# Optimization experiments

Measured on AMD Instinct MI355X. Metric: run time of the kernel, lower is better.

Reference implementation:

```python
import jax, jax.numpy as jnp
import numpy as np

B, M, D = 8, 1024, 768          # batch, tokens, model dim
N, P = 32, 32                   # experts, slots per expert (N*P == M)
K = 8                           # mix_k (router top-k)
H = 2048                        # expert MLP hidden dim
EPS = 1e-12


def setup_inputs() -> dict:
    key = jax.random.key(0)
    ks = jax.random.split(key, 6)
    std_d = 1.0 / np.sqrt(D)
    std_h = 1.0 / np.sqrt(H)
    return {
        "x": jax.random.normal(ks[0], (B, M, D), jnp.float32),
        "cluster_assignments": jax.random.randint(ks[1], (B, M, K), 0, N),
        "phi": jax.random.normal(ks[2], (D, N, P), jnp.float32) * std_d,
        "scale": jnp.ones((1,), jnp.float32),
        "w1": jax.random.normal(ks[3], (N, D, H), jnp.float32) * std_d,
        "b1": jnp.zeros((N, H), jnp.float32),
        "w2": jax.random.normal(ks[4], (N, H, D), jnp.float32) * std_h,
        "b2": jnp.zeros((N, D), jnp.float32),
    }


def _seg_mean(vals, idx, num_segments):
    # index_reduce(..., 'mean', include_self=False): empty segments stay 0
    s = jax.ops.segment_sum(vals, idx, num_segments=num_segments)
    c = jax.ops.segment_sum(jnp.ones((vals.shape[0], 1), vals.dtype), idx,
                            num_segments=num_segments)
    return jnp.where(c > 0, s / jnp.maximum(c, 1.0), 0.0)


def _compute_acmoe(x_flat, top_assign):
    # MAD-based per-cluster, per-dim scaling (mad=True, mix_weights=False)
    mean_kd = _seg_mean(x_flat, top_assign, N)                 # [N, D]
    centered = jnp.abs(x_flat - mean_kd[top_assign])           # [B*M, D]
    w_mad = _seg_mean(centered, top_assign, N)                 # [N, D]
    W = 1.0 / (w_mad + 0.35)
    top_clamp = 5.0 * W.mean()
    W = jnp.minimum(W, top_clamp)
    W = W / W.mean()
    return W[top_assign]                                       # [B*M, D]


def reference(x, cluster_assignments, phi, scale, w1, b1, w2, b2):
    # normalize tokens (dim=2) and phi (dim=0), scale phi
    xn = x / jnp.maximum(jnp.linalg.norm(x, axis=-1, keepdims=True), EPS)
    phin = scale * phi / jnp.maximum(jnp.linalg.norm(phi, axis=0, keepdims=True), EPS)

    # ACMoE feature re-weighting (no-grad in original)
    top_assign = cluster_assignments.reshape(-1, K)[:, 0]       # [B*M]
    Mw = jax.lax.stop_gradient(_compute_acmoe(
        jax.lax.stop_gradient(xn.reshape(-1, D)), top_assign))
    xn = (xn.reshape(-1, D) * Mw).reshape(B, M, D)

    logits = jnp.einsum('bmd,dnp->bmnp', xn, phin)              # [B,M,N,P]
    aff = logits.reshape(B, M, N * P)
    mixing_weights, slot_assignments = jax.lax.top_k(aff, K)    # [B,M,K]
    new_clusters = slot_assignments // P

    disp = jax.nn.softmax(logits, axis=1)                       # over tokens m
    comb = jax.nn.softmax(aff, axis=-1).reshape(B, M, N, P)     # over (n,p)

    xs = jnp.einsum('bmd,bmnp->bnpd', xn, disp)                 # [B,N,P,D]
    # per-expert MLP, batched over expert axis n
    h = jnp.einsum('bnpd,ndh->bnph', xs, w1) + b1[None, :, None, :]
    h = jax.nn.gelu(h, approximate=False)
    ys = jnp.einsum('bnph,nhd->bnpd', h, w2) + b2[None, :, None, :]

    y = jnp.einsum('bnpd,bmnp->bmd', ys, comb)                  # [B,M,D]
    return y, mixing_weights, new_clusters
```

## Files before the change

### kernel.cpp

```cpp
#include <hip/hip_runtime.h>
#include <cmath>

#define NB    8
#define MTOK  1024
#define BMT   8192
#define DD    768
#define NEXP  32
#define PSLOT 32
#define NP    1024
#define KTOP  8
#define HH    2048

#define SLICES 128
#define TPS    64

typedef unsigned short ushort;
typedef __attribute__((ext_vector_type(8))) short short8v;
typedef __attribute__((ext_vector_type(4))) short short4v;
typedef __attribute__((ext_vector_type(4))) float f32x4;

__device__ __forceinline__ ushort bf16_rne(float x) {
    unsigned u = __float_as_uint(x);
    unsigned r = (u + 0x7FFFu + ((u >> 16) & 1u)) >> 16;
    return (ushort)r;
}
__device__ __forceinline__ float bf16_to_f(ushort h) {
    return __uint_as_float(((unsigned)h) << 16);
}
__device__ __forceinline__ void split2(float x, ushort& hi, ushort& lo) {
    hi = bf16_rne(x);
    lo = bf16_rne(x - bf16_to_f(hi));
}
__device__ __forceinline__ unsigned cvt_pk_bf16(float a, float b) {
    unsigned r;
    asm volatile("v_cvt_pk_bf16_f32 %0, %1, %2" : "=v"(r) : "v"(a), "v"(b));
    return r;
}

__device__ __forceinline__ void gl_lds16(const ushort* g, ushort* l) {
    __builtin_amdgcn_global_load_lds(
        (const __attribute__((address_space(1))) void*)g,
        (__attribute__((address_space(3))) void*)l, 16, 0, 0);
}

__global__ __launch_bounds__(256) void norm_x(const float* __restrict__ x, float* __restrict__ xn) {
    int tok = blockIdx.x;
    int t = threadIdx.x;
    const float* p = x + (long)tok * DD;
    float v0 = p[t], v1 = p[t + 256], v2 = p[t + 512];
    float ss = v0 * v0 + v1 * v1 + v2 * v2;
#pragma unroll
    for (int o = 32; o; o >>= 1) ss += __shfl_xor(ss, o);
    __shared__ float sred[4];
    if ((t & 63) == 0) sred[t >> 6] = ss;
    __syncthreads();
    ss = sred[0] + sred[1] + sred[2] + sred[3];
    float inv = 1.0f / fmaxf(sqrtf(ss), 1e-12f);
    float* q = xn + (long)tok * DD;
    q[t] = v0 * inv; q[t + 256] = v1 * inv; q[t + 512] = v2 * inv;
}

__global__ __launch_bounds__(256) void norm_phi_T(const float* __restrict__ phi, const float* __restrict__ scale,
                                                  ushort* __restrict__ phT_hi, ushort* __restrict__ phT_lo) {
    int np = blockIdx.x;
    int t = threadIdx.x;
    float ss = 0.f;
    for (int d = t; d < DD; d += 256) {
        float v = phi[(long)d * NP + np];
        ss += v * v;
    }
#pragma unroll
    for (int o = 32; o; o >>= 1) ss += __shfl_xor(ss, o);
    __shared__ float sred[4];
    if ((t & 63) == 0) sred[t >> 6] = ss;
    __syncthreads();
    ss = sred[0] + sred[1] + sred[2] + sred[3];
    float sc = scale[0] / fmaxf(sqrtf(ss), 1e-12f);
    for (int d = t; d < DD; d += 256) {
        float v = phi[(long)d * NP + np] * sc;
        ushort h, l; split2(v, h, l);
        phT_hi[(long)np * DD + d] = h;
        phT_lo[(long)np * DD + d] = l;
    }
}

__global__ __launch_bounds__(256) void cluster_sum(const float* __restrict__ xn, const int* __restrict__ ca,
                                                   float* __restrict__ spart, float* __restrict__ cntpart) {
    __shared__ float s[NEXP][256];
    __shared__ float cnt[NEXP];
    int chunk = blockIdx.x, slice = blockIdx.y, t = threadIdx.x;
#pragma unroll
    for (int n = 0; n < NEXP; ++n) s[n][t] = 0.f;
    if (t < NEXP) cnt[t] = 0.f;
    __syncthreads();
    int tok0 = slice * TPS;
    for (int i = 0; i < TPS; ++i) {
        int tok = tok0 + i;
        int a = ca[tok * KTOP];
        float v = xn[(long)tok * DD + chunk * 256 + t];
        s[a][t] += v;
        if (chunk == 0 && t == 0) cnt[a] += 1.f;
    }
    __syncthreads();
    for (int n = 0; n < NEXP; ++n)
        spart[(long)slice * (NEXP * DD) + n * DD + chunk * 256 + t] = s[n][t];
    if (chunk == 0 && t < NEXP) cntpart[slice * NEXP + t] = cnt[t];
}

__global__ __launch_bounds__(256) void reduce_parts(const float* __restrict__ part, float* __restrict__ outv,
                                                    const float* __restrict__ cntpart, float* __restrict__ ccnt,
                                                    int doCnt) {
    int i = blockIdx.x * 256 + threadIdx.x;
    float s = 0.f;
#pragma unroll 8
    for (int sl = 0; sl < SLICES; ++sl) s += part[(long)sl * (NEXP * DD) + i];
    outv[i] = s;
    if (doCnt && i < NEXP) {
        float c = 0.f;
#pragma unroll 8
        for (int sl = 0; sl < SLICES; ++sl) c += cntpart[sl * NEXP + i];
        ccnt[i] = c;
    }
}

__global__ __launch_bounds__(256) void cluster_mad(const float* __restrict__ xn, const int* __restrict__ ca,
                                                   const float* __restrict__ csum, const float* __restrict__ ccnt,
                                                   float* __restrict__ mpart) {
    __shared__ float md[NEXP][256];
    __shared__ float mean[NEXP][256];
    int chunk = blockIdx.x, slice = blockIdx.y, t = threadIdx.x;
#pragma unroll
    for (int n = 0; n < NEXP; ++n) {
        float c = ccnt[n];
        mean[n][t] = (c > 0.f) ? csum[n * DD + chunk * 256 + t] / c : 0.f;
        md[n][t] = 0.f;
    }
    __syncthreads();
    int tok0 = slice * TPS;
    for (int i = 0; i < TPS; ++i) {
        int tok = tok0 + i;
        int a = ca[tok * KTOP];
        float v = xn[(long)tok * DD + chunk * 256 + t];
        md[a][t] += fabsf(v - mean[a][t]);
    }
    __syncthreads();
    for (int n = 0; n < NEXP; ++n)
        mpart[(long)slice * (NEXP * DD) + n * DD + chunk * 256 + t] = md[n][t];
}

__global__ __launch_bounds__(1024) void compute_W(const float* __restrict__ cmad, const float* __restrict__ ccnt,
                                                  float* __restrict__ W) {
    __shared__ float s[16];
    int t = threadIdx.x;
    auto block_sum = [&](float v) -> float {
#pragma unroll
        for (int o = 32; o; o >>= 1) v += __shfl_xor(v, o);
        if ((t & 63) == 0) s[t >> 6] = v;
        __syncthreads();
        float tot = 0.f;
#pragma unroll
        for (int i = 0; i < 16; ++i) tot += s[i];
        __syncthreads();
        return tot;
    };
    const int TOT = NEXP * DD;
    float p = 0.f;
    for (int i = t; i < TOT; i += 1024) {
        int n = i / DD;
        float c = ccnt[n];
        float wm = (c > 0.f) ? cmad[i] / c : 0.f;
        p += 1.f / (wm + 0.35f);
    }
    float mean1 = block_sum(p) / (float)TOT;
    float clamp = 5.f * mean1;
    p = 0.f;
    for (int i = t; i < TOT; i += 1024) {
        int n = i / DD;
        float c = ccnt[n];
        float wm = (c > 0.f) ? cmad[i] / c : 0.f;
        p += fminf(1.f / (wm + 0.35f), clamp);
    }
    float mean2 = block_sum(p) / (float)TOT;
    float inv2 = 1.f / mean2;
    for (int i = t; i < TOT; i += 1024) {
        int n = i / DD;
        float c = ccnt[n];
        float wm = (c > 0.f) ? cmad[i] / c : 0.f;
        W[i] = fminf(1.f / (wm + 0.35f), clamp) * inv2;
    }
}

__global__ __launch_bounds__(192) void apply_W(float* __restrict__ xn, const int* __restrict__ ca,
                                               const float* __restrict__ W,
                                               ushort* __restrict__ hi, ushort* __restrict__ lo) {
    int tok = blockIdx.x;
    long d4 = (long)tok * DD + threadIdx.x * 4;
    int a = ca[tok * KTOP];
    float4 v = *reinterpret_cast<float4*>(xn + d4);
    float4 w = *reinterpret_cast<const float4*>(W + a * DD + threadIdx.x * 4);
    v.x *= w.x; v.y *= w.y; v.z *= w.z; v.w *= w.w;
    *reinterpret_cast<float4*>(xn + d4) = v;
    ushort h0,h1,h2,h3,l0,l1,l2,l3;
    split2(v.x,h0,l0); split2(v.y,h1,l1); split2(v.z,h2,l2); split2(v.w,h3,l3);
    *reinterpret_cast<short4v*>(hi + d4) = short4v{(short)h0,(short)h1,(short)h2,(short)h3};
    *reinterpret_cast<short4v*>(lo + d4) = short4v{(short)l0,(short)l1,(short)l2,(short)l3};
}

template <bool F32>
__global__ __launch_bounds__(256) void make_T(const void* __restrict__ srcv, ushort* __restrict__ dst,
                                              int R, int C) {
    __shared__ ushort tile[64][65];
    int z = blockIdx.z;
    int c0 = blockIdx.x * 64, r0 = blockIdx.y * 64;
    int tr = threadIdx.x >> 4;
    int tc4 = (threadIdx.x & 15) * 4;
    long base = (long)z * R * C;
#pragma unroll
    for (int i = 0; i < 4; ++i) {
        int r = tr + i * 16;
        if constexpr (F32) {
            const float* s = (const float*)srcv;
            float4 v = *reinterpret_cast<const float4*>(s + base + (long)(r0 + r) * C + c0 + tc4);
            tile[r][tc4 + 0] = bf16_rne(v.x); tile[r][tc4 + 1] = bf16_rne(v.y);
            tile[r][tc4 + 2] = bf16_rne(v.z); tile[r][tc4 + 3] = bf16_rne(v.w);
        } else {
            const ushort* s = (const ushort*)srcv;
            short4v v = *reinterpret_cast<const short4v*>(s + base + (long)(r0 + r) * C + c0 + tc4);
            tile[r][tc4 + 0] = (ushort)v.x; tile[r][tc4 + 1] = (ushort)v.y;
            tile[r][tc4 + 2] = (ushort)v.z; tile[r][tc4 + 3] = (ushort)v.w;
        }
    }
    __syncthreads();
#pragma unroll
    for (int i = 0; i < 4; ++i) {
        int oc = tr + i * 16;
        short4v o = short4v{(short)tile[tc4 + 0][oc], (short)tile[tc4 + 1][oc],
                            (short)tile[tc4 + 2][oc], (short)tile[tc4 + 3][oc]};
        *reinterpret_cast<short4v*>(dst + base + (long)(c0 + oc) * R + r0 + tc4) = o;
    }
}

template <int MODE, int AMAP, int EPI, bool CBF16, int CMAP>
__global__ __launch_bounds__(256) void gemm2(
    const ushort* __restrict__ Ah_g, const ushort* __restrict__ Al_g,
    const float*  __restrict__ Bf_g,
    const ushort* __restrict__ Bh_g, const ushort* __restrict__ Bl_g,
    float* __restrict__ Cf, ushort* __restrict__ Cb,
    int K, int lda, int ldb, int ldc,
    long sA, long sB, long sC,
    const float* __restrict__ bias, int biasStride) {
    constexpr bool PAIR = (MODE == 1);
    constexpr int BUFS = PAIR ? 12288 : 8192;
    constexpr int BM   = PAIR ? 64 : 128;
    constexpr int MI   = PAIR ? 2 : 4;
    __shared__ __attribute__((aligned(16))) ushort lds[3 * BUFS];

    int orig = blockIdx.x + gridDim.x * (blockIdx.y + gridDim.y * blockIdx.z);
    int nwg = gridDim.x * gridDim.y * gridDim.z;
    int wg = (orig & 7) * (nwg >> 3) + (orig >> 3);
    int bx = wg % gridDim.x;
    int rest = wg / gridDim.x;
    int by = rest % gridDim.y;
    int z  = rest / gridDim.y;
    const int m0 = by * BM;
    const int n0 = bx * 128;

    const int tid = threadIdx.x, lane = tid & 63, w = tid >> 6;
    const int wr = w >> 1, wc = w & 1;
    const int lr = lane & 15, kh = lane >> 4;

    const int NCA = PAIR ? 1 : 2;
    long arowA[2]; int kOffA[2];
#pragma unroll
    for (int i = 0; i < NCA; ++i) {
        int c = i * 256 + tid;
        int r = c >> 2, sp = c & 3;
        kOffA[i] = (sp ^ ((r >> 1) & 3)) << 3;
        int rg = m0 + r;
        if constexpr (AMAP == 0) arowA[i] = (long)z * sA + (long)rg * lda;
        else arowA[i] = ((long)(rg >> 5) * 1024 + (long)z * 32 + (rg & 31)) * (long)lda;
    }
    long browB[2]; int kOffB[2];
#pragma unroll
    for (int i = 0; i < 2; ++i) {
        int c = i * 256 + tid;
        int r = c >> 2, sp = c & 3;
        kOffB[i] = (sp ^ ((r >> 1) & 3)) << 3;
        browB[i] = (long)z * sB + (long)(n0 + r) * ldb;
    }
    const int kq = tid & 7, nq = tid >> 3;

    f32x4 acc[MI][4];
#pragma unroll
    for (int i = 0; i < MI; ++i)
#pragma unroll
        for (int j = 0; j < 4; ++j) acc[i][j] = (f32x4)(0.f);

    auto stageA = [&](int buf, int kk0) {
        const int bb = buf * BUFS;
        if constexpr (MODE == 1) {
            gl_lds16(Ah_g + arowA[0] + kk0 + kOffA[0], &lds[bb + (w * 64) * 8]);
            gl_lds16(Al_g + arowA[0] + kk0 + kOffA[0], &lds[bb + 2048 + (w * 64) * 8]);
#pragma unroll
            for (int i = 0; i < 2; ++i) {
                int base = bb + 4096 + (i * 256 + w * 64) * 8;
                gl_lds16(Bh_g + browB[i] + kk0 + kOffB[i], &lds[base]);
                gl_lds16(Bl_g + browB[i] + kk0 + kOffB[i], &lds[base + 4096]);
            }
        } else if constexpr (MODE == 0) {
#pragma unroll
            for (int i = 0; i < 2; ++i)
                gl_lds16(Ah_g + arowA[i] + kk0 + kOffA[i], &lds[bb + (i * 256 + w * 64) * 8]);
#pragma unroll
            for (int i = 0; i < 2; ++i)
                gl_lds16(Bh_g + browB[i] + kk0 + kOffB[i], &lds[bb + 4096 + (i * 256 + w * 64) * 8]);
        } else {
#pragma unroll
            for (int i = 0; i < 2; ++i)
                gl_lds16(Ah_g + arowA[i] + kk0 + kOffA[i], &lds[bb + (i * 256 + w * 64) * 8]);
        }
    };

    auto loadB = [&](float4 (&rB)[4], int kk0) {
#pragma unroll
        for (int dk = 0; dk < 4; ++dk)
            rB[dk] = *reinterpret_cast<const float4*>(
                Bf_g + (long)z * sB + (long)(kk0 + kq * 4 + dk) * ldb + n0 + nq * 4);
    };

    auto bwrite = [&](int buf, float4 (&rB)[4]) {
        unsigned p0[4], p1[4];
        p0[0] = cvt_pk_bf16(rB[0].x, rB[1].x); p1[0] = cvt_pk_bf16(rB[2].x, rB[3].x);
        p0[1] = cvt_pk_bf16(rB[0].y, rB[1].y); p1[1] = cvt_pk_bf16(rB[2].y, rB[3].y);
        p0[2] = cvt_pk_bf16(rB[0].z, rB[1].z); p1[2] = cvt_pk_bf16(rB[2].z, rB[3].z);
        p0[3] = cvt_pk_bf16(rB[0].w, rB[1].w); p1[3] = cvt_pk_bf16(rB[2].w, rB[3].w);
#pragma unroll
        for (int dn = 0; dn < 4; ++dn) {
            int n = nq * 4 + dn;
            int phys = (kq >> 1) ^ ((n >> 1) & 3);
            int off = buf * BUFS + 4096 + n * 32 + phys * 8 + (kq & 1) * 4;
            *reinterpret_cast<uint2*>(&lds[off]) = make_uint2(p0[dn], p1[dn]);
        }
    };

    auto compute = [&](int buf) {
        const int aB = buf * BUFS;
        const int bB = buf * BUFS + 4096;
        short8v bh[4], bl[4];
#pragma unroll
        for (int nj = 0; nj < 4; ++nj) {
            int rb = wc * 64 + nj * 16 + lr;
            int off = bB + rb * 32 + ((kh ^ ((rb >> 1) & 3)) << 3);
            bh[nj] = *reinterpret_cast<const short8v*>(&lds[off]);
            if constexpr (PAIR) bl[nj] = *reinterpret_cast<const short8v*>(&lds[off + 4096]);
        }
        __builtin_amdgcn_s_setprio(1);
#pragma unroll
        for (int mi = 0; mi < MI; ++mi) {
            int ra = wr * (PAIR ? 32 : 64) + mi * 16 + lr;
            int off = aB + ra * 32 + ((kh ^ ((ra >> 1) & 3)) << 3);
            short8v ah = *reinterpret_cast<const short8v*>(&lds[off]);
            if constexpr (PAIR) {
                short8v al = *reinterpret_cast<const short8v*>(&lds[off + 2048]);
#pragma unroll
                for (int nj = 0; nj < 4; ++nj) {
                    acc[mi][nj] = __builtin_amdgcn_mfma_f32_16x16x32_bf16(ah, bh[nj], acc[mi][nj], 0, 0, 0);
                    acc[mi][nj] = __builtin_amdgcn_mfma_f32_16x16x32_bf16(ah, bl[nj], acc[mi][nj], 0, 0, 0);
                    acc[mi][nj] = __builtin_amdgcn_mfma_f32_16x16x32_bf16(al, bh[nj], acc[mi][nj], 0, 0, 0);
                }
            } else {
#pragma unroll
                for (int nj = 0; nj < 4; ++nj)
                    acc[mi][nj] = __builtin_amdgcn_mfma_f32_16x16x32_bf16(ah, bh[nj], acc[mi][nj], 0, 0, 0);
            }
        }
        __builtin_amdgcn_s_setprio(0);
    };

    const int nt = K >> 5;
    if constexpr (MODE == 0 || MODE == 1) {
        stageA(0, 0);
        stageA(1, 32);
        if constexpr (MODE == 1) { asm volatile("s_waitcnt vmcnt(6)" ::: "memory"); }
        else                     { asm volatile("s_waitcnt vmcnt(4)" ::: "memory"); }
        __builtin_amdgcn_s_barrier();
        __builtin_amdgcn_sched_barrier(0);
        int cc = 0, cn2 = 2;
        for (int t = 0; t < nt; ++t) {
            bool deep = (t + 2 < nt);
            if (deep) stageA(cn2, (t + 2) << 5);
            compute(cc);
            if (deep) {
                if constexpr (MODE == 1) { asm volatile("s_waitcnt vmcnt(6)" ::: "memory"); }
                else                     { asm volatile("s_waitcnt vmcnt(4)" ::: "memory"); }
            } else {
                asm volatile("s_waitcnt vmcnt(0)" ::: "memory");
            }
            if (t + 1 < nt) {
                __builtin_amdgcn_s_barrier();
                __builtin_amdgcn_sched_barrier(0);
            }
            cc = (cc == 2) ? 0 : cc + 1;
            cn2 = (cn2 == 2) ? 0 : cn2 + 1;
        }
    } else {
        float4 rBa[4], rBb[4];
        loadB(rBa, 0);
        bwrite(0, rBa);
        stageA(0, 0);
        stageA(1, 32);
        loadB(rBb, 32);
        asm volatile("s_waitcnt vmcnt(6) lgkmcnt(0)" ::: "memory");
        __builtin_amdgcn_s_barrier();
        __builtin_amdgcn_sched_barrier(0);
        int cc = 0, cn1 = 1, cn2 = 2;
        auto iter = [&](int t, float4 (&ld)[4], float4 (&wr_)[4]) {
            bool deep = (t + 2 < nt);
            if (deep) { stageA(cn2, (t + 2) << 5); loadB(ld, (t + 2) << 5); }
            compute(cc);
            if (t + 1 < nt) bwrite(cn1, wr_);
            if (deep) { asm volatile("s_waitcnt vmcnt(6) lgkmcnt(0)" ::: "memory"); }
            else      { asm volatile("s_waitcnt vmcnt(0) lgkmcnt(0)" ::: "memory"); }
            if (t + 1 < nt) {
                __builtin_amdgcn_s_barrier();
                __builtin_amdgcn_sched_barrier(0);
            }
            cc = (cc == 2) ? 0 : cc + 1;
            cn1 = (cn1 == 2) ? 0 : cn1 + 1;
            cn2 = (cn2 == 2) ? 0 : cn2 + 1;
        };
        for (int t = 0; t < nt; t += 2) {
            iter(t, rBa, rBb);
            iter(t + 1, rBb, rBa);
        }
    }

#pragma unroll
    for (int mi = 0; mi < MI; ++mi)
#pragma unroll
        for (int j = 0; j < 4; ++j) {
            int rg = m0 + wr * (PAIR ? 32 : 64) + mi * 16 + kh * 4 + j;
            long roff;
            if constexpr (CMAP == 1) roff = ((long)(rg >> 5) * 1024 + (long)z * 32 + (rg & 31)) * (long)ldc;
            else                     roff = (long)z * sC + (long)rg * ldc;
#pragma unroll
            for (int nj = 0; nj < 4; ++nj) {
                int col = n0 + wc * 64 + nj * 16 + lr;
                float v = acc[mi][nj][j];
                if constexpr (EPI >= 1) v += bias[(long)z * biasStride + col];
                if constexpr (EPI == 2) v = 0.5f * v * (1.0f + erff(v * 0.70710678118654752f));
                if constexpr (CBF16) Cb[roff + col] = bf16_rne(v);
                else                 Cf[roff + col] = v;
            }
        }
}

__global__ __launch_bounds__(64) void row_topk(const float* __restrict__ logits,
                                               float* __restrict__ mix_out, float* __restrict__ clus_out,
                                               ushort* __restrict__ comb) {
    int row = blockIdx.x;
    int lane = threadIdx.x;
    const float* p = logits + (long)row * NP;
    float v[16];
#pragma unroll
    for (int i = 0; i < 16; ++i) v[i] = p[lane + i * 64];
    float mx = v[0];
#pragma unroll
    for (int i = 1; i < 16; ++i) mx = fmaxf(mx, v[i]);
#pragma unroll
    for (int o = 32; o; o >>= 1) mx = fmaxf(mx, __shfl_xor(mx, o));
    float s = 0.f;
#pragma unroll
    for (int i = 0; i < 16; ++i) s += __expf(v[i] - mx);
#pragma unroll
    for (int o = 32; o; o >>= 1) s += __shfl_xor(s, o);
    float inv = 1.0f / s;
    ushort* crow = comb + (long)row * NP;
#pragma unroll
    for (int i = 0; i < 16; ++i)
        crow[lane + i * 64] = bf16_rne(__expf(v[i] - mx) * inv);
#pragma unroll
    for (int k = 0; k < KTOP; ++k) {
        float bv = -INFINITY; int bi = 1 << 30;
#pragma unroll
        for (int i = 0; i < 16; ++i) {
            if (v[i] > bv) { bv = v[i]; bi = lane + i * 64; }
        }
#pragma unroll
        for (int o = 32; o; o >>= 1) {
            float ov = __shfl_xor(bv, o); int oi = __shfl_xor(bi, o);
            if (ov > bv || (ov == bv && oi < bi)) { bv = ov; bi = oi; }
        }
        int owner = bi & 63, slot = bi >> 6;
        if (lane == owner) {
#pragma unroll
            for (int i = 0; i < 16; ++i) if (slot == i) v[i] = -INFINITY;
        }
        if (lane == k) {
            mix_out[(long)row * KTOP + k] = bv;
            clus_out[(long)row * KTOP + k] = (float)(bi >> 5);
        }
    }
}

__global__ __launch_bounds__(256) void col_stats_part(const float* __restrict__ logits,
                                                      float* __restrict__ pmax, float* __restrict__ psum) {
    int b = blockIdx.z, ms = blockIdx.y, npc = blockIdx.x;
    int np = npc * 256 + threadIdx.x;
    const float* p = logits + ((long)b * MTOK + ms * 128) * NP + np;
    float mx = -INFINITY, s = 0.f;
    for (int m = 0; m < 128; ++m) {
        float v = p[(long)m * NP];
        float nm = fmaxf(mx, v);
        s = s * __expf(mx - nm) + __expf(v - nm);
        mx = nm;
    }
    long o = ((long)b * 8 + ms) * NP + np;
    pmax[o] = mx; psum[o] = s;
}

__global__ __launch_bounds__(256) void make_dispT(const float* __restrict__ logits,
                                                  const float* __restrict__ pmax, const float* __restrict__ psum,
                                                  ushort* __restrict__ dispT) {
    __shared__ float tile[64][65];
    __shared__ float smax[64], sinv[64];
    int b = blockIdx.z, np0 = blockIdx.x * 64, m0 = blockIdx.y * 64;
    int tr = threadIdx.x >> 6, tc = threadIdx.x & 63;
    if (threadIdx.x < 64) {
        int np = np0 + threadIdx.x;
        float mx = -INFINITY;
#pragma unroll
        for (int ms = 0; ms < 8; ++ms) mx = fmaxf(mx, pmax[((long)b * 8 + ms) * NP + np]);
        float s = 0.f;
#pragma unroll
        for (int ms = 0; ms < 8; ++ms) {
            long o = ((long)b * 8 + ms) * NP + np;
            s += psum[o] * __expf(pmax[o] - mx);
        }
        smax[threadIdx.x] = mx;
        sinv[threadIdx.x] = 1.0f / s;
    }
    const float* src = logits + ((long)b * MTOK + m0) * NP + np0;
#pragma unroll
    for (int i = 0; i < 16; ++i) {
        int m = tr * 16 + i;
        tile[m][tc] = src[(long)m * NP + tc];
    }
    __syncthreads();
#pragma unroll
    for (int i = 0; i < 16; ++i) {
        int npl = tr * 16 + i;
        float v = __expf(tile[tc][npl] - smax[npl]) * sinv[npl];
        dispT[((long)b * NP + np0 + npl) * MTOK + (m0 + tc)] = bf16_rne(v);
    }
}

extern "C" void kernel_launch(void* const* d_in, const int* in_sizes, int n_in,
                              void* d_out, int out_size, void* d_ws, size_t ws_size,
                              hipStream_t stream) {
    const float* x    = (const float*)d_in[0];
    const int*   ca   = (const int*)d_in[1];
    const float* phi  = (const float*)d_in[2];
    const float* scale= (const float*)d_in[3];
    const float* w1   = (const float*)d_in[4];
    const float* b1   = (const float*)d_in[5];
    const float* w2   = (const float*)d_in[6];
    const float* b2   = (const float*)d_in[7];
    float* out = (float*)d_out;
    float* ws  = (float*)d_ws;

    float*  xn       = ws;
    float*  logits   = xn + 6291456;
    ushort* xnp_hi   = (ushort*)(logits + 8388608);
    ushort* xnp_lo   = xnp_hi + 6291456;
    ushort* phT_hi   = xnp_lo + 6291456;
    ushort* phT_lo   = phT_hi + 786432;
    ushort* dispT_bf = phT_lo + 786432;
    ushort* comb_bf  = dispT_bf + 8388608;
    ushort* xs_bf    = comb_bf + 8388608;
    ushort* h_bf     = xs_bf + 6291456;
    ushort* xnT_bf   = h_bf + 16777216;
    ushort* ysT_bf   = xnT_bf + 6291456;
    float*  stats    = (float*)(ysT_bf + 6291456);
    float* pmax      = stats;
    float* psum      = pmax + 65536;
    float* csum      = psum + 65536;
    float* cmad      = csum + 24576;
    float* Wbuf      = cmad + 24576;
    float* ccnt      = Wbuf + 24576;
    float* cntpart   = ccnt + 64;
    float* spart     = cntpart + 4096;
    float* mpart     = spart + 3145728;
    float* ys        = xn;

    float* out_y    = out;
    float* out_mix  = out + 6291456;
    float* out_clus = out + 6291456 + 65536;

    norm_x<<<BMT, 256, 0, stream>>>(x, xn);
    norm_phi_T<<<NP, 256, 0, stream>>>(phi, scale, phT_hi, phT_lo);

    cluster_sum<<<dim3(3, SLICES), 256, 0, stream>>>(xn, ca, spart, cntpart);
    reduce_parts<<<96, 256, 0, stream>>>(spart, csum, cntpart, ccnt, 1);
    cluster_mad<<<dim3(3, SLICES), 256, 0, stream>>>(xn, ca, csum, ccnt, mpart);
    reduce_parts<<<96, 256, 0, stream>>>(mpart, cmad, nullptr, nullptr, 0);
    compute_W<<<1, 1024, 0, stream>>>(cmad, ccnt, Wbuf);
    apply_W<<<BMT, 192, 0, stream>>>(xn, ca, Wbuf, xnp_hi, xnp_lo);

    make_T<false><<<dim3(12, 16, NB), 256, 0, stream>>>(xnp_hi, xnT_bf, MTOK, DD);

    gemm2<1, 0, 0, false, 0><<<dim3(8, 128, 1), 256, 0, stream>>>(
        xnp_hi, xnp_lo, nullptr, phT_hi, phT_lo, logits, nullptr,
        DD, DD, DD, NP, 0, 0, 0, nullptr, 0);

    row_topk<<<BMT, 64, 0, stream>>>(logits, out_mix, out_clus, comb_bf);
    col_stats_part<<<dim3(4, 8, NB), 256, 0, stream>>>(logits, pmax, psum);
    make_dispT<<<dim3(16, 16, NB), 256, 0, stream>>>(logits, pmax, psum, dispT_bf);

    gemm2<0, 0, 0, true, 0><<<dim3(6, 8, NB), 256, 0, stream>>>(
        dispT_bf, nullptr, nullptr, xnT_bf, nullptr, nullptr, xs_bf,
        MTOK, MTOK, MTOK, DD,
        (long)NP * MTOK, (long)DD * MTOK, (long)NP * DD, nullptr, 0);

    gemm2<2, 1, 2, true, 0><<<dim3(16, 2, NEXP), 256, 0, stream>>>(
        xs_bf, nullptr, w1, nullptr, nullptr, nullptr, h_bf,
        DD, DD, HH, HH,
        0, (long)DD * HH, (long)256 * HH, b1, HH);

    gemm2<2, 0, 1, false, 1><<<dim3(6, 2, NEXP), 256, 0, stream>>>(
        h_bf, nullptr, w2, nullptr, nullptr, ys, nullptr,
        HH, HH, DD, DD,
        (long)256 * HH, (long)HH * DD, 0, b2, DD);

    make_T<true><<<dim3(12, 16, NB), 256, 0, stream>>>(ys, ysT_bf, MTOK, DD);

    gemm2<0, 0, 0, false, 0><<<dim3(6, 8, NB), 256, 0, stream>>>(
        comb_bf, nullptr, nullptr, ysT_bf, nullptr, out_y, nullptr,
        NP, NP, NP, DD,
        (long)MTOK * NP, (long)DD * NP, (long)MTOK * DD, nullptr, 0);
}
```

Before: 478.4 us.

## Double M tile to 256 rows with 512-thread blocks in bf16 GEMMs

For the non-paired GEMM modes, the workgroup grows to 512 threads and covers 256 output rows instead of 128. Each B tile staged in LDS is now shared by twice as many rows, which halves B traffic per output and halves the grid size. B staging and fp32→bf16 conversion are remapped to the new thread count, the vmcnt waits are adjusted, and the s_setprio hints around the MFMA loop are dropped. The trade-off is fewer workgroups: some launches fall to 192 blocks, which can leave CUs idle, and the larger blocks limit occupancy.

```diff
diff --git a/kernel.cpp b/kernel.cpp
--- a/kernel.cpp
+++ b/kernel.cpp
@@ -241,7 +241,7 @@
 }
 
 template <int MODE, int AMAP, int EPI, bool CBF16, int CMAP>
-__global__ __launch_bounds__(256) void gemm2(
+__global__ __launch_bounds__((MODE == 1) ? 256 : 512) void gemm2(
     const ushort* __restrict__ Ah_g, const ushort* __restrict__ Al_g,
     const float*  __restrict__ Bf_g,
     const ushort* __restrict__ Bh_g, const ushort* __restrict__ Bl_g,
@@ -250,8 +250,10 @@
     long sA, long sB, long sC,
     const float* __restrict__ bias, int biasStride) {
     constexpr bool PAIR = (MODE == 1);
-    constexpr int BUFS = PAIR ? 12288 : 8192;
-    constexpr int BM   = PAIR ? 64 : 128;
+    constexpr int THR  = PAIR ? 256 : 512;
+    constexpr int BUFS = 12288;
+    constexpr int BOFF = PAIR ? 4096 : 8192;
+    constexpr int BM   = PAIR ? 64 : 256;
     constexpr int MI   = PAIR ? 2 : 4;
     __shared__ __attribute__((aligned(16))) ushort lds[3 * BUFS];
 
@@ -273,7 +275,7 @@
     long arowA[2]; int kOffA[2];
 #pragma unroll
     for (int i = 0; i < NCA; ++i) {
-        int c = i * 256 + tid;
+        int c = i * THR + tid;
         int r = c >> 2, sp = c & 3;
         kOffA[i] = (sp ^ ((r >> 1) & 3)) << 3;
         int rg = m0 + r;
@@ -284,11 +286,13 @@
 #pragma unroll
     for (int i = 0; i < 2; ++i) {
         int c = i * 256 + tid;
-        int r = c >> 2, sp = c & 3;
-        kOffB[i] = (sp ^ ((r >> 1) & 3)) << 3;
-        browB[i] = (long)z * sB + (long)(n0 + r) * ldb;
-    }
-    const int kq = tid & 7, nq = tid >> 3;
+        if (c < 512) {
+            int r = c >> 2, sp = c & 3;
+            kOffB[i] = (sp ^ ((r >> 1) & 3)) << 3;
+            browB[i] = (long)z * sB + (long)(n0 + r) * ldb;
+        }
+    }
+    const int kqh = tid & 15, nq = tid >> 4;
 
     f32x4 acc[MI][4];
 #pragma unroll
@@ -310,42 +314,42 @@
         } else if constexpr (MODE == 0) {
 #pragma unroll
             for (int i = 0; i < 2; ++i)
-                gl_lds16(Ah_g + arowA[i] + kk0 + kOffA[i], &lds[bb + (i * 256 + w * 64) * 8]);
+                gl_lds16(Ah_g + arowA[i] + kk0 + kOffA[i], &lds[bb + (i * THR + w * 64) * 8]);
+            gl_lds16(Bh_g + browB[0] + kk0 + kOffB[0], &lds[bb + BOFF + (w * 64) * 8]);
+        } else {
 #pragma unroll
             for (int i = 0; i < 2; ++i)
-                gl_lds16(Bh_g + browB[i] + kk0 + kOffB[i], &lds[bb + 4096 + (i * 256 + w * 64) * 8]);
-        } else {
-#pragma unroll
-            for (int i = 0; i < 2; ++i)
-                gl_lds16(Ah_g + arowA[i] + kk0 + kOffA[i], &lds[bb + (i * 256 + w * 64) * 8]);
+                gl_lds16(Ah_g + arowA[i] + kk0 + kOffA[i], &lds[bb + (i * THR + w * 64) * 8]);
         }
     };
 
-    auto loadB = [&](float4 (&rB)[4], int kk0) {
-#pragma unroll
-        for (int dk = 0; dk < 4; ++dk)
+    auto loadB = [&](float4 (&rB)[2], int kk0) {
+#pragma unroll
+        for (int dk = 0; dk < 2; ++dk)
             rB[dk] = *reinterpret_cast<const float4*>(
-                Bf_g + (long)z * sB + (long)(kk0 + kq * 4 + dk) * ldb + n0 + nq * 4);
+                Bf_g + (long)z * sB + (long)(kk0 + kqh * 2 + dk) * ldb + n0 + nq * 4);
     };
 
-    auto bwrite = [&](int buf, float4 (&rB)[4]) {
-        unsigned p0[4], p1[4];
-        p0[0] = cvt_pk_bf16(rB[0].x, rB[1].x); p1[0] = cvt_pk_bf16(rB[2].x, rB[3].x);
-        p0[1] = cvt_pk_bf16(rB[0].y, rB[1].y); p1[1] = cvt_pk_bf16(rB[2].y, rB[3].y);
-        p0[2] = cvt_pk_bf16(rB[0].z, rB[1].z); p1[2] = cvt_pk_bf16(rB[2].z, rB[3].z);
-        p0[3] = cvt_pk_bf16(rB[0].w, rB[1].w); p1[3] = cvt_pk_bf16(rB[2].w, rB[3].w);
+    auto bwrite = [&](int buf, float4 (&rB)[2]) {
+        unsigned p[4];
+        p[0] = cvt_pk_bf16(rB[0].x, rB[1].x);
+        p[1] = cvt_pk_bf16(rB[0].y, rB[1].y);
+        p[2] = cvt_pk_bf16(rB[0].z, rB[1].z);
+        p[3] = cvt_pk_bf16(rB[0].w, rB[1].w);
+        int k = kqh * 2;
+        int s = k >> 3, kin = k & 7;
 #pragma unroll
         for (int dn = 0; dn < 4; ++dn) {
             int n = nq * 4 + dn;
-            int phys = (kq >> 1) ^ ((n >> 1) & 3);
-            int off = buf * BUFS + 4096 + n * 32 + phys * 8 + (kq & 1) * 4;
-            *reinterpret_cast<uint2*>(&lds[off]) = make_uint2(p0[dn], p1[dn]);
+            int phys = s ^ ((n >> 1) & 3);
+            int off = buf * BUFS + BOFF + n * 32 + phys * 8 + kin;
+            *reinterpret_cast<unsigned*>(&lds[off]) = p[dn];
         }
     };
 
     auto compute = [&](int buf) {
         const int aB = buf * BUFS;
-        const int bB = buf * BUFS + 4096;
+        const int bB = buf * BUFS + BOFF;
         short8v bh[4], bl[4];
 #pragma unroll
         for (int nj = 0; nj < 4; ++nj) {
@@ -354,7 +358,6 @@
             bh[nj] = *reinterpret_cast<const short8v*>(&lds[off]);
             if constexpr (PAIR) bl[nj] = *reinterpret_cast<const short8v*>(&lds[off + 4096]);
         }
-        __builtin_amdgcn_s_setprio(1);
 #pragma unroll
         for (int mi = 0; mi < MI; ++mi) {
             int ra = wr * (PAIR ? 32 : 64) + mi * 16 + lr;
@@ -374,7 +377,6 @@
                     acc[mi][nj] = __builtin_amdgcn_mfma_f32_16x16x32_bf16(ah, bh[nj], acc[mi][nj], 0, 0, 0);
             }
         }
-        __builtin_amdgcn_s_setprio(0);
     };
 
     const int nt = K >> 5;
@@ -382,7 +384,7 @@
         stageA(0, 0);
         stageA(1, 32);
         if constexpr (MODE == 1) { asm volatile("s_waitcnt vmcnt(6)" ::: "memory"); }
-        else                     { asm volatile("s_waitcnt vmcnt(4)" ::: "memory"); }
+        else                     { asm volatile("s_waitcnt vmcnt(3)" ::: "memory"); }
         __builtin_amdgcn_s_barrier();
         __builtin_amdgcn_sched_barrier(0);
         int cc = 0, cn2 = 2;
@@ -392,7 +394,7 @@
             compute(cc);
             if (deep) {
                 if constexpr (MODE == 1) { asm volatile("s_waitcnt vmcnt(6)" ::: "memory"); }
-                else                     { asm volatile("s_waitcnt vmcnt(4)" ::: "memory"); }
+                else                     { asm volatile("s_waitcnt vmcnt(3)" ::: "memory"); }
             } else {
                 asm volatile("s_waitcnt vmcnt(0)" ::: "memory");
             }
@@ -404,22 +406,22 @@
             cn2 = (cn2 == 2) ? 0 : cn2 + 1;
         }
     } else {
-        float4 rBa[4], rBb[4];
+        float4 rBa[2], rBb[2];
         loadB(rBa, 0);
         bwrite(0, rBa);
         stageA(0, 0);
         stageA(1, 32);
         loadB(rBb, 32);
-        asm volatile("s_waitcnt vmcnt(6) lgkmcnt(0)" ::: "memory");
+        asm volatile("s_waitcnt vmcnt(4) lgkmcnt(0)" ::: "memory");
         __builtin_amdgcn_s_barrier();
         __builtin_amdgcn_sched_barrier(0);
         int cc = 0, cn1 = 1, cn2 = 2;
-        auto iter = [&](int t, float4 (&ld)[4], float4 (&wr_)[4]) {
+        auto iter = [&](int t, float4 (&ld)[2], float4 (&wr_)[2]) {
             bool deep = (t + 2 < nt);
             if (deep) { stageA(cn2, (t + 2) << 5); loadB(ld, (t + 2) << 5); }
             compute(cc);
             if (t + 1 < nt) bwrite(cn1, wr_);
-            if (deep) { asm volatile("s_waitcnt vmcnt(6) lgkmcnt(0)" ::: "memory"); }
+            if (deep) { asm volatile("s_waitcnt vmcnt(4) lgkmcnt(0)" ::: "memory"); }
             else      { asm volatile("s_waitcnt vmcnt(0) lgkmcnt(0)" ::: "memory"); }
             if (t + 1 < nt) {
                 __builtin_amdgcn_s_barrier();
@@ -617,24 +619,24 @@
     col_stats_part<<<dim3(4, 8, NB), 256, 0, stream>>>(logits, pmax, psum);
     make_dispT<<<dim3(16, 16, NB), 256, 0, stream>>>(logits, pmax, psum, dispT_bf);
 
-    gemm2<0, 0, 0, true, 0><<<dim3(6, 8, NB), 256, 0, stream>>>(
+    gemm2<0, 0, 0, true, 0><<<dim3(6, 4, NB), 512, 0, stream>>>(
         dispT_bf, nullptr, nullptr, xnT_bf, nullptr, nullptr, xs_bf,
         MTOK, MTOK, MTOK, DD,
         (long)NP * MTOK, (long)DD * MTOK, (long)NP * DD, nullptr, 0);
 
-    gemm2<2, 1, 2, true, 0><<<dim3(16, 2, NEXP), 256, 0, stream>>>(
+    gemm2<2, 1, 2, true, 0><<<dim3(16, 1, NEXP), 512, 0, stream>>>(
         xs_bf, nullptr, w1, nullptr, nullptr, nullptr, h_bf,
         DD, DD, HH, HH,
         0, (long)DD * HH, (long)256 * HH, b1, HH);
 
-    gemm2<2, 0, 1, false, 1><<<dim3(6, 2, NEXP), 256, 0, stream>>>(
+    gemm2<2, 0, 1, false, 1><<<dim3(6, 1, NEXP), 512, 0, stream>>>(
         h_bf, nullptr, w2, nullptr, nullptr, ys, nullptr,
         HH, HH, DD, DD,
         (long)256 * HH, (long)HH * DD, 0, b2, DD);
 
     make_T<true><<<dim3(12, 16, NB), 256, 0, stream>>>(ys, ysT_bf, MTOK, DD);
 
-    gemm2<0, 0, 0, false, 0><<<dim3(6, 8, NB), 256, 0, stream>>>(
+    gemm2<0, 0, 0, false, 0><<<dim3(6, 4, NB), 512, 0, stream>>>(
         comb_bf, nullptr, nullptr, ysT_bf, nullptr, out_y, nullptr,
         NP, NP, NP, DD,
         (long)MTOK * NP, (long)DD * NP, (long)MTOK * DD, nullptr, 0);
```

Measured after the change: 466.1 us. 2.6% less time.
